# Optimization experiments

Hardware: AMD Instinct MI355X
Metric: run time of the kernel (lower is better)

## Reference

```python
import jax, jax.numpy as jnp
import numpy as np

HIDDEN = 4096
N_HEADS = 32
N_KV_HEADS = 8
HEAD_DIM = HIDDEN // N_HEADS  # 128
GROUPS = N_HEADS // N_KV_HEADS  # 4
B, S = 1, 2048
NEG = -1e9


def setup_inputs() -> dict:
    key = jax.random.key(0)
    ks = jax.random.split(key, 8)
    hidden_states = jax.random.normal(ks[0], (B, S, HIDDEN), dtype=jnp.float32)
    # additive causal mask [B,1,S,S]
    causal = jnp.tril(jnp.ones((S, S), dtype=bool))
    attention_mask = jnp.where(causal, 0.0, NEG).astype(jnp.float32)[None, None]
    position_ids = jnp.broadcast_to(jnp.arange(S, dtype=jnp.int64), (B, S))
    inv_freq = 1.0 / (500000.0 ** (np.arange(0, HEAD_DIM, 2, dtype=np.float32) / HEAD_DIM))
    freqs = np.arange(S, dtype=np.float32)[:, None] * inv_freq[None, :]  # [S, 64]
    cos = jnp.asarray(np.cos(freqs), dtype=jnp.float32)
    sin = jnp.asarray(np.sin(freqs), dtype=jnp.float32)
    sc = 1.0 / np.sqrt(HIDDEN)
    Wq = jax.random.normal(ks[1], (HIDDEN, HIDDEN), dtype=jnp.float32) * sc
    Wk = jax.random.normal(ks[2], (N_KV_HEADS * HEAD_DIM, HIDDEN), dtype=jnp.float32) * sc
    Wv = jax.random.normal(ks[3], (N_KV_HEADS * HEAD_DIM, HIDDEN), dtype=jnp.float32) * sc
    Wo = jax.random.normal(ks[4], (HIDDEN, HIDDEN), dtype=jnp.float32) * sc
    return {"hidden_states": hidden_states, "attention_mask": attention_mask,
            "position_ids": position_ids, "cos": cos, "sin": sin,
            "Wq": Wq, "Wk": Wk, "Wv": Wv, "Wo": Wo}


def _rope(q, k, cos, sin, position_ids):
    # cos/sin: [max_pos, head_dim//2]; gather per position -> [b,1,s,hd/2]
    c = cos[position_ids][:, None]  # [b,1,s,d/2]
    s_ = sin[position_ids][:, None]
    q1, q2 = q[..., ::2], q[..., 1::2]
    k1, k2 = k[..., ::2], k[..., 1::2]
    q_rot = jnp.concatenate([q1 * c - q2 * s_, q2 * c + q1 * s_], axis=-1)
    k_rot = jnp.concatenate([k1 * c - k2 * s_, k2 * c + k1 * s_], axis=-1)
    return q_rot, k_rot


def reference(hidden_states, attention_mask, position_ids, cos, sin, Wq, Wk, Wv, Wo):
    b, s, _ = hidden_states.shape
    q = jnp.einsum('bsh,oh->bso', hidden_states, Wq).reshape(b, s, N_HEADS, HEAD_DIM).transpose(0, 2, 1, 3)
    k = jnp.einsum('bsh,oh->bso', hidden_states, Wk).reshape(b, s, N_KV_HEADS, HEAD_DIM).transpose(0, 2, 1, 3)
    v = jnp.einsum('bsh,oh->bso', hidden_states, Wv).reshape(b, s, N_KV_HEADS, HEAD_DIM).transpose(0, 2, 1, 3)
    q, k = _rope(q, k, cos, sin, position_ids)
    if GROUPS > 1:
        k = jnp.repeat(k, GROUPS, axis=1)  # [b,H,s,d]
        v = jnp.repeat(v, GROUPS, axis=1)
    scores = jnp.einsum('bhqd,bhkd->bhqk', q, k) / np.sqrt(HEAD_DIM)
    scores = scores + attention_mask
    attn = jax.nn.softmax(scores.astype(jnp.float32), axis=-1).astype(q.dtype)
    out = jnp.einsum('bhqk,bhkd->bhqd', attn, v)
    out = out.transpose(0, 2, 1, 3).reshape(b, s, HIDDEN)
    out = jnp.einsum('bso,ho->bsh', out, Wo)
    return out
```

## Files before the change

kernel.cpp:

```cpp
#include <hip/hip_runtime.h>
#include <hip/hip_bf16.h>

#define S_LEN 2048
#define HID   4096
#define NH    32
#define NKV   8
#define HD    128

typedef __attribute__((ext_vector_type(8))) short short8v;
typedef __attribute__((ext_vector_type(4))) float floatx4;

__device__ __forceinline__ float bf2f(unsigned short u) {
  union { unsigned int u32; float f; } v; v.u32 = ((unsigned int)u) << 16; return v.f;
}
__device__ __forceinline__ unsigned short f2bf(float f) {
  union { float f; unsigned int u; } v; v.f = f;
  unsigned int u = v.u + 0x7fffu + ((v.u >> 16) & 1u);
  return (unsigned short)(u >> 16);
}
__device__ __forceinline__ unsigned int cvtpk_bf16(float lo, float hi) {
  unsigned int r;
  asm("v_cvt_pk_bf16_f32 %0, %1, %2" : "=v"(r) : "v"(lo), "v"(hi));
  return r;
}

__device__ __forceinline__ void gld_lds16(const void* g, void* l) {
  __builtin_amdgcn_global_load_lds((const __attribute__((address_space(1))) void*)g,
                                   (__attribute__((address_space(3))) void*)l, 16, 0, 0);
}

__global__ __launch_bounds__(256) void cvt_all(const float* __restrict__ X,  const float* __restrict__ Wq,
                                               const float* __restrict__ Wk, const float* __restrict__ Wv,
                                               const float* __restrict__ Wo,
                                               unsigned short* __restrict__ Xb,  unsigned short* __restrict__ Wqb,
                                               unsigned short* __restrict__ Wkb, unsigned short* __restrict__ Wvb,
                                               unsigned short* __restrict__ Wob) {
  const int c0 = 2097152;
  const int c1 = c0 + 4194304;
  const int c2 = c1 + 1048576;
  const int c3 = c2 + 1048576;
  const int c4 = c3 + 4194304;
  int i = blockIdx.x * blockDim.x + threadIdx.x;
  int stride = gridDim.x * blockDim.x;
  for (; i < c4; i += stride) {
    const float* src; unsigned short* dst; int off;
    if (i < c0)      { src = X;  dst = Xb;  off = i; }
    else if (i < c1) { src = Wq; dst = Wqb; off = i - c0; }
    else if (i < c2) { src = Wk; dst = Wkb; off = i - c1; }
    else if (i < c3) { src = Wv; dst = Wvb; off = i - c2; }
    else             { src = Wo; dst = Wob; off = i - c3; }
    float4 v = ((const float4*)src)[off];
    ushort4 o;
    o.x = f2bf(v.x); o.y = f2bf(v.y); o.z = f2bf(v.z); o.w = f2bf(v.w);
    ((ushort4*)dst)[off] = o;
  }
}

__device__ __forceinline__ void gemm256_core(const unsigned short* __restrict__ A,
                                             const unsigned short* __restrict__ B,
                                             unsigned short* lds,
                                             int brow, int bcol, int tid,
                                             floatx4 acc[8][4]) {
  const int K = 4096;
  const int w = tid >> 6, lane = tid & 63;
  const int fr = lane & 15, fq = lane >> 4;
  const int wm = w >> 2, wn = w & 3;

  const int r0s = w * 32 + (lane >> 2);
  const int r1s = r0s + 16;
  const int sl0 = ((lane & 3) ^ ((r0s >> 1) & 3)) << 3;
  const int sl1 = ((lane & 3) ^ ((r1s >> 1) & 3)) << 3;
  const unsigned short* pAs0 = A + (size_t)(brow + r0s) * K + sl0;
  const unsigned short* pAs1 = A + (size_t)(brow + r1s) * K + sl1;
  const unsigned short* pBs0 = B + (size_t)(bcol + r0s) * K + sl0;
  const unsigned short* pBs1 = B + (size_t)(bcol + r1s) * K + sl1;

  const int sl = (fq ^ ((fr >> 1) & 3)) << 3;
  int aoffb[8], boffb[4];
#pragma unroll
  for (int m = 0; m < 8; ++m) aoffb[m] = (wm * 128 + m * 16 + fr) * 32 + sl;
#pragma unroll
  for (int n = 0; n < 4; ++n) boffb[n] = 16384 + (wn * 64 + n * 16 + fr) * 32 + sl;

#define STG_A(buf, kh, t)                                                     \
  do {                                                                        \
    const int ko_ = (t) * 64 + (kh) * 32;                                     \
    gld_lds16(pAs0 + ko_, lds + (buf) * 32768 + (kh) * 8192 + w * 1024);      \
    gld_lds16(pAs1 + ko_, lds + (buf) * 32768 + (kh) * 8192 + w * 1024 + 512);\
  } while (0)
#define STG_B(buf, kh, t)                                                     \
  do {                                                                        \
    const int ko_ = (t) * 64 + (kh) * 32;                                     \
    gld_lds16(pBs0 + ko_, lds + (buf) * 32768 + 16384 + (kh) * 8192 + w * 1024);      \
    gld_lds16(pBs1 + ko_, lds + (buf) * 32768 + 16384 + (kh) * 8192 + w * 1024 + 512);\
  } while (0)

#define LGKM0_FENCE                                                \
  asm volatile("s_waitcnt lgkmcnt(0)" ::: "memory");               \
  __builtin_amdgcn_sched_barrier(0)

  STG_A(0, 0, 0); STG_B(0, 0, 0);
  STG_A(0, 1, 0); STG_B(0, 1, 0);
  STG_A(1, 0, 1); STG_B(1, 0, 1);
  asm volatile("s_waitcnt vmcnt(8)" ::: "memory");
  __builtin_amdgcn_s_barrier();

  const int NT = K / 64;
  for (int t = 0; t < NT; ++t) {
    const int c = t & 1;
    const unsigned short* Lc = lds + c * 32768;
    short8v a_[4], b_[4], a2_[4];

#pragma unroll
    for (int m = 0; m < 4; ++m) a_[m] = *(const short8v*)&Lc[aoffb[m]];
#pragma unroll
    for (int n = 0; n < 4; ++n) b_[n] = *(const short8v*)&Lc[boffb[n]];
    if (t + 1 < NT) STG_A(c ^ 1, 1, t + 1);
    __builtin_amdgcn_s_barrier();
    LGKM0_FENCE;
    __builtin_amdgcn_s_setprio(1);
#pragma unroll
    for (int m = 0; m < 4; ++m)
#pragma unroll
      for (int n = 0; n < 4; ++n)
        acc[m][n] = __builtin_amdgcn_mfma_f32_16x16x32_bf16(a_[m], b_[n], acc[m][n], 0, 0, 0);
    __builtin_amdgcn_s_setprio(0);
    __builtin_amdgcn_s_barrier();

#pragma unroll
    for (int m = 0; m < 4; ++m) a2_[m] = *(const short8v*)&Lc[aoffb[m + 4]];
    if (t + 1 < NT) STG_B(c ^ 1, 1, t + 1);
    __builtin_amdgcn_s_barrier();
    LGKM0_FENCE;
    __builtin_amdgcn_s_setprio(1);
#pragma unroll
    for (int m = 0; m < 4; ++m)
#pragma unroll
      for (int n = 0; n < 4; ++n)
        acc[m + 4][n] = __builtin_amdgcn_mfma_f32_16x16x32_bf16(a2_[m], b_[n], acc[m + 4][n], 0, 0, 0);
    __builtin_amdgcn_s_setprio(0);
    if (t == NT - 1) asm volatile("s_waitcnt vmcnt(0)" ::: "memory");
    else             asm volatile("s_waitcnt vmcnt(8)" ::: "memory");
    __builtin_amdgcn_s_barrier();

#pragma unroll
    for (int m = 0; m < 4; ++m) a_[m] = *(const short8v*)&Lc[8192 + aoffb[m]];
#pragma unroll
    for (int n = 0; n < 4; ++n) b_[n] = *(const short8v*)&Lc[8192 + boffb[n]];
    if (t + 2 < NT) STG_A(c, 0, t + 2);
    __builtin_amdgcn_s_barrier();
    LGKM0_FENCE;
    __builtin_amdgcn_s_setprio(1);
#pragma unroll
    for (int m = 0; m < 4; ++m)
#pragma unroll
      for (int n = 0; n < 4; ++n)
        acc[m][n] = __builtin_amdgcn_mfma_f32_16x16x32_bf16(a_[m], b_[n], acc[m][n], 0, 0, 0);
    __builtin_amdgcn_s_setprio(0);
    __builtin_amdgcn_s_barrier();

#pragma unroll
    for (int m = 0; m < 4; ++m) a2_[m] = *(const short8v*)&Lc[8192 + aoffb[m + 4]];
    if (t + 2 < NT) STG_B(c, 0, t + 2);
    __builtin_amdgcn_s_barrier();
    LGKM0_FENCE;
    __builtin_amdgcn_s_setprio(1);
#pragma unroll
    for (int m = 0; m < 4; ++m)
#pragma unroll
      for (int n = 0; n < 4; ++n)
        acc[m + 4][n] = __builtin_amdgcn_mfma_f32_16x16x32_bf16(a2_[m], b_[n], acc[m + 4][n], 0, 0, 0);
    __builtin_amdgcn_s_setprio(0);
    if (t >= NT - 2) asm volatile("s_waitcnt vmcnt(0)" ::: "memory");
    else             asm volatile("s_waitcnt vmcnt(8)" ::: "memory");
    __builtin_amdgcn_s_barrier();
  }
#undef STG_A
#undef STG_B
#undef LGKM0_FENCE
}

__global__ __launch_bounds__(512, 2) void gemm_qkv(const unsigned short* __restrict__ Xb,
                                                   const unsigned short* __restrict__ Wqb,
                                                   const unsigned short* __restrict__ Wkb,
                                                   const unsigned short* __restrict__ Wvb,
                                                   unsigned short* __restrict__ Qg,
                                                   unsigned short* __restrict__ Kg,
                                                   unsigned short* __restrict__ Vt) {
  __shared__ unsigned short lds[2 * 32768];
  const int bx = blockIdx.x;
  const unsigned short* B; unsigned short* C; int mode, bcol, ldc;
  if (bx < 16)      { B = Wqb; C = Qg; mode = 0; bcol = bx * 256;        ldc = HID;  }
  else if (bx < 20) { B = Wkb; C = Kg; mode = 0; bcol = (bx - 16) * 256; ldc = 1024; }
  else              { B = Wvb; C = Vt; mode = 1; bcol = (bx - 20) * 256; ldc = 0;    }
  const int brow = blockIdx.y * 256;
  const int tid = threadIdx.x;
  floatx4 acc[8][4] = {};
  gemm256_core(Xb, B, lds, brow, bcol, tid, acc);

  const int w = tid >> 6, lane = tid & 63;
  const int fr = lane & 15, fq = lane >> 4;
  const int wm = w >> 2, wn = w & 3;
  const int r0 = brow + wm * 128 + fq * 4;
  const int c0 = bcol + wn * 64 + fr;
  if (mode == 0) {
#pragma unroll
    for (int m = 0; m < 8; ++m)
#pragma unroll
      for (int n = 0; n < 4; ++n)
#pragma unroll
        for (int r = 0; r < 4; ++r)
          C[(size_t)(r0 + m * 16 + r) * ldc + c0 + n * 16] = f2bf(acc[m][n][r]);
  } else {
#pragma unroll
    for (int m = 0; m < 8; ++m)
#pragma unroll
      for (int n = 0; n < 4; ++n) {
        ushort4 pk;
        pk.x = f2bf(acc[m][n][0]); pk.y = f2bf(acc[m][n][1]);
        pk.z = f2bf(acc[m][n][2]); pk.w = f2bf(acc[m][n][3]);
        *(ushort4*)&Vt[(size_t)(c0 + n * 16) * S_LEN + (r0 + m * 16)] = pk;
      }
  }
}

__global__ __launch_bounds__(512, 2) void gemm_o(const unsigned short* __restrict__ Ao,
                                                 const unsigned short* __restrict__ Wob,
                                                 float* __restrict__ Out) {
  __shared__ unsigned short lds[2 * 24576];
  const int K = 4096;
  const int tid = threadIdx.x;
  const int w = tid >> 6, lane = tid & 63;
  const int fr = lane & 15, fq = lane >> 4;
  const int wm = w >> 1, wn = w & 1;
  const int brow = blockIdx.y * 256, bcol = blockIdx.x * 128;

  const int rA = tid >> 2;
  const int sA = ((tid & 3) ^ ((rA >> 1) & 3)) << 3;
  const unsigned short* pA0 = Ao  + (size_t)(brow + rA) * K + sA;
  const unsigned short* pA1 = Ao  + (size_t)(brow + 128 + rA) * K + sA;
  const unsigned short* pB0 = Wob + (size_t)(bcol + rA) * K + sA;

  const int sl = (fq ^ ((fr >> 1) & 3)) << 3;
  int aoff[4], boff[4];
#pragma unroll
  for (int m = 0; m < 4; ++m) aoff[m] = (wm * 64 + m * 16 + fr) * 32 + sl;
#pragma unroll
  for (int n = 0; n < 4; ++n) boff[n] = 16384 + (wn * 64 + n * 16 + fr) * 32 + sl;

  floatx4 acc[4][4] = {};

#define STG_KH(buf, kh, t)                                                       \
  do {                                                                           \
    const int ko_ = (t) * 64 + (kh) * 32;                                        \
    gld_lds16(pA0 + ko_, lds + (buf) * 24576 + (kh) * 8192 + w * 512);           \
    gld_lds16(pA1 + ko_, lds + (buf) * 24576 + (kh) * 8192 + 4096 + w * 512);    \
    gld_lds16(pB0 + ko_, lds + (buf) * 24576 + 16384 + (kh) * 4096 + w * 512);   \
  } while (0)

  STG_KH(0, 0, 0);
  STG_KH(0, 1, 0);
  STG_KH(1, 0, 1);
  asm volatile("s_waitcnt vmcnt(6)" ::: "memory");
  __builtin_amdgcn_s_barrier();

  const int NT = K / 64;
  for (int t = 0; t < NT; ++t) {
    const int c = t & 1;
    const unsigned short* Lc = lds + c * 24576;
    short8v a_[4], b_[4];

#pragma unroll
    for (int m = 0; m < 4; ++m) a_[m] = *(const short8v*)&Lc[aoff[m]];
#pragma unroll
    for (int n = 0; n < 4; ++n) b_[n] = *(const short8v*)&Lc[boff[n]];
    if (t + 1 < NT) STG_KH(c ^ 1, 1, t + 1);
    __builtin_amdgcn_s_setprio(1);
#pragma unroll
    for (int m = 0; m < 4; ++m)
#pragma unroll
      for (int n = 0; n < 4; ++n)
        acc[m][n] = __builtin_amdgcn_mfma_f32_16x16x32_bf16(a_[m], b_[n], acc[m][n], 0, 0, 0);
    __builtin_amdgcn_s_setprio(0);
    if (t + 1 < NT) asm volatile("s_waitcnt vmcnt(6)" ::: "memory");
    else            asm volatile("s_waitcnt vmcnt(0)" ::: "memory");
    __builtin_amdgcn_s_barrier();

#pragma unroll
    for (int m = 0; m < 4; ++m) a_[m] = *(const short8v*)&Lc[8192 + aoff[m]];
#pragma unroll
    for (int n = 0; n < 4; ++n) b_[n] = *(const short8v*)&Lc[4096 + boff[n]];
    if (t + 2 < NT) STG_KH(c, 0, t + 2);
    __builtin_amdgcn_s_setprio(1);
#pragma unroll
    for (int m = 0; m < 4; ++m)
#pragma unroll
      for (int n = 0; n < 4; ++n)
        acc[m][n] = __builtin_amdgcn_mfma_f32_16x16x32_bf16(a_[m], b_[n], acc[m][n], 0, 0, 0);
    __builtin_amdgcn_s_setprio(0);
    if (t + 2 < NT)      asm volatile("s_waitcnt vmcnt(6)" ::: "memory");
    else if (t + 1 < NT) asm volatile("s_waitcnt vmcnt(3)" ::: "memory");
    else                 asm volatile("s_waitcnt vmcnt(0)" ::: "memory");
    __builtin_amdgcn_s_barrier();
  }
#undef STG_KH

  const int r0 = brow + wm * 64 + fq * 4;
  const int c0 = bcol + wn * 64 + fr;
#pragma unroll
  for (int m = 0; m < 4; ++m)
#pragma unroll
    for (int n = 0; n < 4; ++n)
#pragma unroll
      for (int r = 0; r < 4; ++r)
        Out[(size_t)(r0 + m * 16 + r) * HID + c0 + n * 16] = acc[m][n][r];
}

__global__ __launch_bounds__(256) void rope_k(const unsigned short* __restrict__ In,
                                              const float* __restrict__ cosT,
                                              const float* __restrict__ sinT,
                                              unsigned short* __restrict__ Out) {
  int idx = blockIdx.x * 256 + threadIdx.x;
  int j = idx & 63;
  int s = (idx >> 6) & (S_LEN - 1);
  int h = idx >> 17;
  unsigned int pr = *(const unsigned int*)(In + (size_t)s * (NKV * HD) + h * HD + 2 * j);
  float k1 = bf2f((unsigned short)(pr & 0xffffu));
  float k2 = bf2f((unsigned short)(pr >> 16));
  float c = cosT[s * 64 + j], sn = sinT[s * 64 + j];
  unsigned int pk = (unsigned int)f2bf(k1 * c - k2 * sn) |
                    ((unsigned int)f2bf(k2 * c + k1 * sn) << 16);
  *(unsigned int*)(Out + ((size_t)h * S_LEN + s) * HD + 2 * j) = pk;
}

__global__ __launch_bounds__(256) void attn_fwd(const unsigned short* __restrict__ Qg,
                                                const float* __restrict__ cosT,
                                                const float* __restrict__ sinT,
                                                const unsigned short* __restrict__ Kr,
                                                const unsigned short* __restrict__ Vt,
                                                unsigned short* __restrict__ Ao) {
  __shared__ unsigned short Kl[2][64 * 128];
  __shared__ unsigned short Vl[2][64 * 128];
  const int id = blockIdx.x;
  const int swz = (id & 7) * 128 + (id >> 3);
  const int h  = swz >> 5;
  const int qt = 31 - (swz & 31);
  const int hk = h >> 2;
  const int qb = qt * 64;
  const int tid = threadIdx.x, w = tid >> 6, lane = tid & 63;
  const int fr = lane & 15, fq = lane >> 4;

  short8v aq[4];
  {
    const int s_row = qb + w * 16 + fr;
    const unsigned short* qp = Qg + (size_t)s_row * HID + h * HD + fq * 8;
    const float* cb = cosT + s_row * 64;
    const float* sb = sinT + s_row * 64;
    const float SC = 0.12751744f;
#pragma unroll
    for (int ks = 0; ks < 4; ++ks) {
      short8v raw = *(const short8v*)(qp + ks * 32);
      short8v ov;
#pragma unroll
      for (int e = 0; e < 4; ++e) {
        float q1 = bf2f((unsigned short)raw[2 * e]);
        float q2 = bf2f((unsigned short)raw[2 * e + 1]);
        int j = ks * 16 + fq * 4 + e;
        float c = cb[j], sn = sb[j];
        ov[2 * e]     = (short)f2bf(SC * (q1 * c - q2 * sn));
        ov[2 * e + 1] = (short)f2bf(SC * (q2 * c + q1 * sn));
      }
      aq[ks] = ov;
    }
  }

  const int kcb = ((tid & 15) * 16) ^ (((tid >> 4) & 7) << 4);
  const unsigned short* pK0 = Kr + ((size_t)hk * S_LEN + (tid >> 4)) * HD + (kcb >> 1);
  const int vcb = ((tid & 7) * 16) ^ (((tid >> 3) & 7) << 4);
  const unsigned short* pV0 = Vt + ((size_t)hk * HD + (tid >> 3)) * S_LEN + (vcb >> 1);

  const int hsel = fq >> 1;
  const int srcA = fr + ((2 * (fq & 1)) << 4);
  const int srcB = fr + ((2 * (fq & 1) + 1) << 4);

  float l_acc = 0.f;
  floatx4 o[8] = {};

#define STAGE(buf, t)                                                          \
  do {                                                                         \
    const unsigned short* pk_ = pK0 + (size_t)(t) * 64 * HD;                   \
    const unsigned short* pv_ = pV0 + (t) * 64;                                \
    _Pragma("unroll")                                                          \
    for (int j = 0; j < 4; ++j)                                                \
      gld_lds16(pk_ + (size_t)j * 16 * HD, &Kl[buf][w * 512 + j * 2048]);      \
    _Pragma("unroll")                                                          \
    for (int j = 0; j < 4; ++j)                                                \
      gld_lds16(pv_ + (size_t)j * 32 * S_LEN, &Vl[buf][w * 512 + j * 2048]);   \
  } while (0)

  STAGE(0, 0);
  asm volatile("s_waitcnt vmcnt(0)" ::: "memory");
  __syncthreads();

  int cur = 0;
  for (int t = 0; t <= qt; ++t) {
    const int kv0 = t * 64;
    if (t < qt) STAGE(cur ^ 1, t + 1);

    floatx4 St[4] = {};
    const unsigned short* Kc = &Kl[cur][0];
    const unsigned short* Vc = &Vl[cur][0];
    __builtin_amdgcn_s_setprio(1);
#pragma unroll
    for (int ks = 0; ks < 4; ++ks) {
#pragma unroll
      for (int n = 0; n < 4; ++n) {
        int row = n * 16 + fr;
        int cb = (ks * 64 + fq * 16) ^ ((row & 7) << 4);
        short8v kf = *(const short8v*)&Kc[row * 128 + (cb >> 1)];
        St[n] = __builtin_amdgcn_mfma_f32_16x16x32_bf16(kf, aq[ks], St[n], 0, 0, 0);
      }
    }
    __builtin_amdgcn_s_setprio(0);

    if (t == qt) {
#pragma unroll
      for (int n = 0; n < 4; ++n) {
#pragma unroll
        for (int r = 0; r < 4; ++r) {
          int kvg = kv0 + n * 16 + fq * 4 + r;
          if (kvg > qb + w * 16 + fr) St[n][r] = -1e30f;
        }
      }
    }

    unsigned int pk[4][2];
#pragma unroll
    for (int n = 0; n < 4; ++n) {
      float p0 = exp2f(St[n][0]);
      float p1 = exp2f(St[n][1]);
      float p2 = exp2f(St[n][2]);
      float p3 = exp2f(St[n][3]);
      l_acc += (p0 + p1) + (p2 + p3);
      pk[n][0] = cvtpk_bf16(p0, p1);
      pk[n][1] = cvtpk_bf16(p2, p3);
    }

    short8v pa[2];
#pragma unroll
    for (int ks = 0; ks < 2; ++ks) {
      unsigned int v0a = __shfl(pk[2 * ks][0], srcA), v0b = __shfl(pk[2 * ks + 1][0], srcA);
      unsigned int v1a = __shfl(pk[2 * ks][1], srcA), v1b = __shfl(pk[2 * ks + 1][1], srcA);
      unsigned int v2a = __shfl(pk[2 * ks][0], srcB), v2b = __shfl(pk[2 * ks + 1][0], srcB);
      unsigned int v3a = __shfl(pk[2 * ks][1], srcB), v3b = __shfl(pk[2 * ks + 1][1], srcB);
      uint4 u;
      u.x = hsel ? v0b : v0a;
      u.y = hsel ? v1b : v1a;
      u.z = hsel ? v2b : v2a;
      u.w = hsel ? v3b : v3a;
      pa[ks] = *(short8v*)&u;
    }

    __builtin_amdgcn_s_setprio(1);
#pragma unroll
    for (int nf = 0; nf < 8; ++nf) {
#pragma unroll
      for (int ks = 0; ks < 2; ++ks) {
        int row = nf * 16 + fr;
        int cb = (ks * 64 + fq * 16) ^ ((row & 7) << 4);
        short8v bv = *(const short8v*)&Vc[row * 64 + (cb >> 1)];
        o[nf] = __builtin_amdgcn_mfma_f32_16x16x32_bf16(pa[ks], bv, o[nf], 0, 0, 0);
      }
    }
    __builtin_amdgcn_s_setprio(0);

    if (t < qt) {
      asm volatile("s_waitcnt vmcnt(0)" ::: "memory");
      __syncthreads();
      cur ^= 1;
    }
  }
#undef STAGE

  float L = l_acc;
  L += __shfl_xor(L, 16);
  L += __shfl_xor(L, 32);
  float rinv[4];
#pragma unroll
  for (int r = 0; r < 4; ++r) rinv[r] = 1.0f / __shfl(L, fq * 4 + r);

  unsigned short* aop = Ao + (size_t)(qb + w * 16 + fq * 4) * HID + h * HD + fr;
#pragma unroll
  for (int nf = 0; nf < 8; ++nf)
#pragma unroll
    for (int r = 0; r < 4; ++r)
      aop[(size_t)r * HID + nf * 16] = f2bf(o[nf][r] * rinv[r]);
}

extern "C" void kernel_launch(void* const* d_in, const int* in_sizes, int n_in,
                              void* d_out, int out_size, void* d_ws, size_t ws_size,
                              hipStream_t stream) {
  (void)in_sizes; (void)n_in; (void)out_size; (void)ws_size;
  const float* X    = (const float*)d_in[0];
  const float* cosT = (const float*)d_in[3];
  const float* sinT = (const float*)d_in[4];
  const float* Wq   = (const float*)d_in[5];
  const float* Wk   = (const float*)d_in[6];
  const float* Wv   = (const float*)d_in[7];
  const float* Wo   = (const float*)d_in[8];

  char* ws = (char*)d_ws;
  size_t off = 0;
  auto alloc = [&](size_t bytes) { char* p = ws + off; off += (bytes + 255) & ~(size_t)255; return p; };
  unsigned short* Xb  = (unsigned short*)alloc((size_t)S_LEN * HID * 2);
  unsigned short* Wqb = (unsigned short*)alloc((size_t)HID * HID * 2);
  unsigned short* Wkb = (unsigned short*)alloc((size_t)1024 * HID * 2);
  unsigned short* Wvb = (unsigned short*)alloc((size_t)1024 * HID * 2);
  unsigned short* Wob = (unsigned short*)alloc((size_t)HID * HID * 2);
  unsigned short* Qg  = (unsigned short*)alloc((size_t)S_LEN * HID * 2);
  unsigned short* Kg  = (unsigned short*)alloc((size_t)S_LEN * 1024 * 2);
  unsigned short* Vt  = (unsigned short*)alloc((size_t)1024 * S_LEN * 2);
  unsigned short* Kr = Wqb;
  unsigned short* Ao = Xb;

  cvt_all<<<2048, 256, 0, stream>>>(X, Wq, Wk, Wv, Wo, Xb, Wqb, Wkb, Wvb, Wob);
  gemm_qkv<<<dim3(24, 8), 512, 0, stream>>>(Xb, Wqb, Wkb, Wvb, Qg, Kg, Vt);
  rope_k<<<(NKV * S_LEN * 64) / 256, 256, 0, stream>>>(Kg, cosT, sinT, Kr);
  attn_fwd<<<1024, 256, 0, stream>>>(Qg, cosT, sinT, Kr, Vt, Ao);
  gemm_o<<<dim3(32, 8), 512, 0, stream>>>(Ao, Wob, (float*)d_out);
}
```

Before: 324.2 us.

## Enlarge attention query tile to 128 rows and drop per-phase GEMM barriers

The attention kernel now uses 512-thread blocks covering 128 query rows, so each staged K/V tile in LDS is shared by twice as many warps and the grid halves. The block-to-head mapping is also reworked so the four query heads sharing a KV head land on the same XCD. Separately, the GEMM main loop drops the intra-iteration s_barrier and lgkmcnt(0) fences before each MFMA phase, leaving ordering of LDS reads to the compiler. Removing those barriers risks LDS read/write races with the async global-to-LDS staging, and the larger causal tiles do more masked work on the diagonal.

New measurement: 293.2 us. 9.6% less time.

```diff
diff --git a/kernel.cpp b/kernel.cpp
--- a/kernel.cpp
+++ b/kernel.cpp
@@ -95,10 +95,6 @@
     gld_lds16(pBs1 + ko_, lds + (buf) * 32768 + 16384 + (kh) * 8192 + w * 1024 + 512);\
   } while (0)
 
-#define LGKM0_FENCE                                                \
-  asm volatile("s_waitcnt lgkmcnt(0)" ::: "memory");               \
-  __builtin_amdgcn_sched_barrier(0)
-
   STG_A(0, 0, 0); STG_B(0, 0, 0);
   STG_A(0, 1, 0); STG_B(0, 1, 0);
   STG_A(1, 0, 1); STG_B(1, 0, 1);
@@ -116,8 +112,6 @@
 #pragma unroll
     for (int n = 0; n < 4; ++n) b_[n] = *(const short8v*)&Lc[boffb[n]];
     if (t + 1 < NT) STG_A(c ^ 1, 1, t + 1);
-    __builtin_amdgcn_s_barrier();
-    LGKM0_FENCE;
     __builtin_amdgcn_s_setprio(1);
 #pragma unroll
     for (int m = 0; m < 4; ++m)
@@ -130,8 +124,6 @@
 #pragma unroll
     for (int m = 0; m < 4; ++m) a2_[m] = *(const short8v*)&Lc[aoffb[m + 4]];
     if (t + 1 < NT) STG_B(c ^ 1, 1, t + 1);
-    __builtin_amdgcn_s_barrier();
-    LGKM0_FENCE;
     __builtin_amdgcn_s_setprio(1);
 #pragma unroll
     for (int m = 0; m < 4; ++m)
@@ -148,8 +140,6 @@
 #pragma unroll
     for (int n = 0; n < 4; ++n) b_[n] = *(const short8v*)&Lc[8192 + boffb[n]];
     if (t + 2 < NT) STG_A(c, 0, t + 2);
-    __builtin_amdgcn_s_barrier();
-    LGKM0_FENCE;
     __builtin_amdgcn_s_setprio(1);
 #pragma unroll
     for (int m = 0; m < 4; ++m)
@@ -162,8 +152,6 @@
 #pragma unroll
     for (int m = 0; m < 4; ++m) a2_[m] = *(const short8v*)&Lc[8192 + aoffb[m + 4]];
     if (t + 2 < NT) STG_B(c, 0, t + 2);
-    __builtin_amdgcn_s_barrier();
-    LGKM0_FENCE;
     __builtin_amdgcn_s_setprio(1);
 #pragma unroll
     for (int m = 0; m < 4; ++m)
@@ -177,7 +165,6 @@
   }
 #undef STG_A
 #undef STG_B
-#undef LGKM0_FENCE
 }
 
 __global__ __launch_bounds__(512, 2) void gemm_qkv(const unsigned short* __restrict__ Xb,
@@ -333,20 +320,20 @@
   *(unsigned int*)(Out + ((size_t)h * S_LEN + s) * HD + 2 * j) = pk;
 }
 
-__global__ __launch_bounds__(256) void attn_fwd(const unsigned short* __restrict__ Qg,
-                                                const float* __restrict__ cosT,
-                                                const float* __restrict__ sinT,
-                                                const unsigned short* __restrict__ Kr,
-                                                const unsigned short* __restrict__ Vt,
-                                                unsigned short* __restrict__ Ao) {
+__global__ __launch_bounds__(512, 4) void attn_fwd(const unsigned short* __restrict__ Qg,
+                                                   const float* __restrict__ cosT,
+                                                   const float* __restrict__ sinT,
+                                                   const unsigned short* __restrict__ Kr,
+                                                   const unsigned short* __restrict__ Vt,
+                                                   unsigned short* __restrict__ Ao) {
   __shared__ unsigned short Kl[2][64 * 128];
-  __shared__ unsigned short Vl[2][64 * 128];
+  __shared__ unsigned short Vl[2][128 * 64];
   const int id = blockIdx.x;
-  const int swz = (id & 7) * 128 + (id >> 3);
-  const int h  = swz >> 5;
-  const int qt = 31 - (swz & 31);
+  const int xcd = id & 7, rr = id >> 3;
+  const int qt = 15 - (rr >> 2);
+  const int h  = xcd * 4 + (rr & 3);
   const int hk = h >> 2;
-  const int qb = qt * 64;
+  const int qb = qt * 128;
   const int tid = threadIdx.x, w = tid >> 6, lane = tid & 63;
   const int fr = lane & 15, fq = lane >> 4;
 
@@ -386,26 +373,27 @@
   float l_acc = 0.f;
   floatx4 o[8] = {};
 
-#define STAGE(buf, t)                                                          \
-  do {                                                                         \
-    const unsigned short* pk_ = pK0 + (size_t)(t) * 64 * HD;                   \
-    const unsigned short* pv_ = pV0 + (t) * 64;                                \
-    _Pragma("unroll")                                                          \
-    for (int j = 0; j < 4; ++j)                                                \
-      gld_lds16(pk_ + (size_t)j * 16 * HD, &Kl[buf][w * 512 + j * 2048]);      \
-    _Pragma("unroll")                                                          \
-    for (int j = 0; j < 4; ++j)                                                \
-      gld_lds16(pv_ + (size_t)j * 32 * S_LEN, &Vl[buf][w * 512 + j * 2048]);   \
+#define STAGE(buf, t)                                                           \
+  do {                                                                          \
+    const unsigned short* pk_ = pK0 + (size_t)(t) * 64 * HD;                    \
+    const unsigned short* pv_ = pV0 + (t) * 64;                                 \
+    _Pragma("unroll")                                                           \
+    for (int j = 0; j < 2; ++j)                                                 \
+      gld_lds16(pk_ + (size_t)j * 32 * HD, &Kl[buf][j * 4096 + w * 512]);       \
+    _Pragma("unroll")                                                           \
+    for (int j = 0; j < 2; ++j)                                                 \
+      gld_lds16(pv_ + (size_t)j * 64 * S_LEN, &Vl[buf][j * 4096 + w * 512]);    \
   } while (0)
 
   STAGE(0, 0);
   asm volatile("s_waitcnt vmcnt(0)" ::: "memory");
   __syncthreads();
 
+  const int nt = 2 * qt + 2;
   int cur = 0;
-  for (int t = 0; t <= qt; ++t) {
+  for (int t = 0; t < nt; ++t) {
     const int kv0 = t * 64;
-    if (t < qt) STAGE(cur ^ 1, t + 1);
+    if (t + 1 < nt) STAGE(cur ^ 1, t + 1);
 
     floatx4 St[4] = {};
     const unsigned short* Kc = &Kl[cur][0];
@@ -423,7 +411,7 @@
     }
     __builtin_amdgcn_s_setprio(0);
 
-    if (t == qt) {
+    if (t >= 2 * qt) {
 #pragma unroll
       for (int n = 0; n < 4; ++n) {
 #pragma unroll
@@ -474,7 +462,7 @@
     }
     __builtin_amdgcn_s_setprio(0);
 
-    if (t < qt) {
+    if (t + 1 < nt) {
       asm volatile("s_waitcnt vmcnt(0)" ::: "memory");
       __syncthreads();
       cur ^= 1;
@@ -526,6 +514,6 @@
   cvt_all<<<2048, 256, 0, stream>>>(X, Wq, Wk, Wv, Wo, Xb, Wqb, Wkb, Wvb, Wob);
   gemm_qkv<<<dim3(24, 8), 512, 0, stream>>>(Xb, Wqb, Wkb, Wvb, Qg, Kg, Vt);
   rope_k<<<(NKV * S_LEN * 64) / 256, 256, 0, stream>>>(Kg, cosT, sinT, Kr);
-  attn_fwd<<<1024, 256, 0, stream>>>(Qg, cosT, sinT, Kr, Vt, Ao);
+  attn_fwd<<<512, 512, 0, stream>>>(Qg, cosT, sinT, Kr, Vt, Ao);
   gemm_o<<<dim3(32, 8), 512, 0, stream>>>(Ao, Wob, (float*)d_out);
 }
```
